# Kernel optimization log

Hardware: AMD Instinct MI355X
Metric: run time of the kernel (lower is better)

Reference implementation:

```python
import jax, jax.numpy as jnp
import numpy as np

D_MODEL = 1024
NUM_HEAD = 16
D_HEAD = 64
EPS = 1e-06


def setup_inputs() -> dict:
    key = jax.random.key(0)
    ks = jax.random.split(key, 16)
    d, h = D_MODEL, 4 * D_MODEL
    s = 1.0 / np.sqrt(d)
    inp = {
        "x": jax.random.normal(ks[0], (8, 1024, d), dtype=jnp.float32),
        # LayerNorm params
        "alpha1": jnp.ones((d,), jnp.float32),
        "beta1": jnp.zeros((d,), jnp.float32),
        "alpha2": jnp.ones((d,), jnp.float32),
        "beta2": jnp.zeros((d,), jnp.float32),
        # attention projections (weights stored as [in, out])
        "w_q": jax.random.normal(ks[1], (d, d), jnp.float32) * s,
        "b_q": jnp.zeros((d,), jnp.float32),
        "w_k": jax.random.normal(ks[2], (d, d), jnp.float32) * s,
        "b_k": jnp.zeros((d,), jnp.float32),
        "w_v": jax.random.normal(ks[3], (d, d), jnp.float32) * s,
        "b_v": jnp.zeros((d,), jnp.float32),
        "w_o": jax.random.normal(ks[4], (d, d), jnp.float32) * s,
        "b_o": jnp.zeros((d,), jnp.float32),
        # MLP
        "w1": jax.random.normal(ks[5], (d, h), jnp.float32) * s,
        "b1": jnp.zeros((h,), jnp.float32),
        "w2": jax.random.normal(ks[6], (h, d), jnp.float32) * (1.0 / np.sqrt(h)),
        "b2": jnp.zeros((d,), jnp.float32),
    }
    return inp


def _layer_norm(x, alpha, beta):
    mu = jnp.mean(x, axis=-1, keepdims=True)
    # torch .var() defaults to unbiased (ddof=1) — replicate exactly
    var = jnp.var(x, axis=-1, keepdims=True, ddof=1)
    return (x - mu) / jnp.sqrt(var + EPS) * alpha + beta


def _mha(x, w_q, b_q, w_k, b_k, w_v, b_v, w_o, b_o):
    b, p, _ = x.shape
    q = (x @ w_q + b_q).reshape(b, p, NUM_HEAD, D_HEAD).transpose(0, 2, 1, 3)
    k = (x @ w_k + b_k).reshape(b, p, NUM_HEAD, D_HEAD).transpose(0, 2, 1, 3)
    v = (x @ w_v + b_v).reshape(b, p, NUM_HEAD, D_HEAD).transpose(0, 2, 1, 3)
    scores = jnp.einsum("bhqd,bhkd->bhqk", q, k) / np.sqrt(D_HEAD).astype(np.float32)
    attn = jax.nn.softmax(scores, axis=-1)
    out = jnp.einsum("bhqk,bhkd->bhqd", attn, v)
    out = out.transpose(0, 2, 1, 3).reshape(b, p, NUM_HEAD * D_HEAD)
    return out @ w_o + b_o


def reference(x, alpha1, beta1, alpha2, beta2,
              w_q, b_q, w_k, b_k, w_v, b_v, w_o, b_o,
              w1, b1, w2, b2):
    # eval mode: Dropout is identity
    x = x + _mha(_layer_norm(x, alpha1, beta1), w_q, b_q, w_k, b_k, w_v, b_v, w_o, b_o)
    h = _layer_norm(x, alpha2, beta2)
    h = jax.nn.gelu(h @ w1 + b1, approximate=False)  # nn.GELU default: exact erf
    h = h @ w2 + b2
    return x + h
```

## Files before the change

kernel.cpp:

```cpp
#include <hip/hip_runtime.h>
#include <stdint.h>

typedef float f32x4 __attribute__((ext_vector_type(4)));
typedef short s16x8 __attribute__((ext_vector_type(8)));
typedef short s16x4 __attribute__((ext_vector_type(4)));
typedef unsigned int u32x4 __attribute__((ext_vector_type(4)));

#define M_TOTAL 8192
#define DM 1024
#define HID 4096
#define SEQ 1024
#define NH 16
#define DH 64

#define BAR() __builtin_amdgcn_s_barrier()
#define VMCNT8() do { asm volatile("s_waitcnt vmcnt(8)" ::: "memory"); __builtin_amdgcn_sched_barrier(0); } while (0)
#define VMCNT0() do { asm volatile("s_waitcnt vmcnt(0)" ::: "memory"); __builtin_amdgcn_sched_barrier(0); } while (0)
#define MFMA16 __builtin_amdgcn_mfma_f32_16x16x32_bf16

__device__ __forceinline__ unsigned short f2bf(float f) {
  unsigned int u = __float_as_uint(f);
  u = (u + 0x7fffu + ((u >> 16) & 1u)) >> 16;
  return (unsigned short)u;
}

__device__ __forceinline__ void gload16(const void* g, void* l) {
  __builtin_amdgcn_global_load_lds((__attribute__((address_space(1))) void*)g,
                                   (__attribute__((address_space(3))) void*)l,
                                   16, 0, 0);
}

__device__ __forceinline__ float erf_fast(float z) {
  const float az = fabsf(z);
  const float tt = 1.0f / fmaf(0.3275911f, az, 1.0f);
  float poly = fmaf(1.061405429f, tt, -1.453152027f);
  poly = fmaf(poly, tt, 1.421413741f);
  poly = fmaf(poly, tt, -0.284496736f);
  poly = fmaf(poly, tt, 0.254829592f);
  poly *= tt;
  const float e = __expf(-az * az);
  const float r = 1.0f - poly * e;
  return (z < 0.f) ? -r : r;
}

__global__ void tcast_all(const float* __restrict__ wq, const float* __restrict__ wk,
                          const float* __restrict__ wv, const float* __restrict__ wo,
                          const float* __restrict__ w1, const float* __restrict__ w2,
                          unsigned short* __restrict__ WTqkv, unsigned short* __restrict__ WTo,
                          unsigned short* __restrict__ WT1, unsigned short* __restrict__ WT2) {
  __shared__ float tile[32][33];
  const int b = blockIdx.x;
  const float* W;
  unsigned short* WT;
  int K, N, bn, bk;
  if (b < 4096) {
    const int j = b >> 10, t2 = b & 1023;
    K = 1024; N = 1024;
    bn = t2 & 31; bk = t2 >> 5;
    W = (j == 0) ? wq : (j == 1) ? wk : (j == 2) ? wv : wo;
    WT = (j < 3) ? (WTqkv + (size_t)j * 1024 * 1024) : WTo;
  } else if (b < 8192) {
    const int t2 = b - 4096;
    K = 1024; N = 4096;
    bn = t2 & 127; bk = t2 >> 7;
    W = w1; WT = WT1;
  } else {
    const int t2 = b - 8192;
    K = 4096; N = 1024;
    bn = t2 & 31; bk = t2 >> 5;
    W = w2; WT = WT2;
  }
  const int tx = threadIdx.x, ty = threadIdx.y;
#pragma unroll
  for (int i = 0; i < 32; i += 8)
    tile[ty + i][tx] = W[(size_t)(bk * 32 + ty + i) * N + bn * 32 + tx];
  __syncthreads();
#pragma unroll
  for (int i = 0; i < 32; i += 8)
    WT[(size_t)(bn * 32 + ty + i) * K + bk * 32 + tx] = f2bf(tile[tx][ty + i]);
}

__global__ __launch_bounds__(256)
void ln_kernel(const float* __restrict__ x, const float* __restrict__ alpha,
               const float* __restrict__ beta, unsigned short* __restrict__ out) {
  const int row = blockIdx.x;
  const int t = threadIdx.x;
  const int w = t >> 6, lane = t & 63;
  const float4 v = ((const float4*)(x + (size_t)row * DM))[t];

  float s = v.x + v.y + v.z + v.w;
#pragma unroll
  for (int off = 32; off; off >>= 1) s += __shfl_xor(s, off, 64);
  __shared__ float red1[4];
  __shared__ float red2[4];
  if (lane == 0) red1[w] = s;
  __syncthreads();
  const float mu = (red1[0] + red1[1] + red1[2] + red1[3]) * (1.f / 1024.f);

  const float dx = v.x - mu, dy = v.y - mu, dz = v.z - mu, dw = v.w - mu;
  float sq = dx * dx + dy * dy + dz * dz + dw * dw;
#pragma unroll
  for (int off = 32; off; off >>= 1) sq += __shfl_xor(sq, off, 64);
  if (lane == 0) red2[w] = sq;
  __syncthreads();
  const float var = (red2[0] + red2[1] + red2[2] + red2[3]) * (1.f / 1023.f);
  const float rstd = rsqrtf(var + 1e-6f);

  const float4 a = ((const float4*)alpha)[t];
  const float4 b = ((const float4*)beta)[t];
  s16x4 o;
  o[0] = (short)f2bf(dx * rstd * a.x + b.x);
  o[1] = (short)f2bf(dy * rstd * a.y + b.y);
  o[2] = (short)f2bf(dz * rstd * a.z + b.z);
  o[3] = (short)f2bf(dw * rstd * a.w + b.w);
  *(s16x4*)(out + (size_t)row * DM + 4 * t) = o;
}

template <int MODE>
__device__ __forceinline__ void epi_store(int m, int n, float v, int Nout,
                                          unsigned short* __restrict__ obf, float* of,
                                          const float* res,
                                          const float* __restrict__ bias0) {
  if (MODE == 1) {
    v += bias0[n] + res[(size_t)m * Nout + n];
    of[(size_t)m * Nout + n] = v;
  } else {
    v += bias0[n];
    const float gv = 0.5f * v * (1.0f + erf_fast(v * 0.70710678118654752f));
    obf[(size_t)m * Nout + n] = f2bf(gv);
  }
}

template <int MODE>
__global__ __launch_bounds__(256, 2)
void gemmk(const unsigned short* __restrict__ A, const unsigned short* __restrict__ B,
           int K, int Nout,
           unsigned short* __restrict__ obf, float* of, const float* res,
           const float* __restrict__ bias0, const float* __restrict__ bias1,
           const float* __restrict__ bias2) {
  __shared__ __attribute__((aligned(16))) unsigned short sA[2][128 * 64];
  __shared__ __attribute__((aligned(16))) unsigned short sB[2][128 * 64];
  const int t = threadIdx.x;
  const int lane = t & 63, wid = t >> 6;
  const int g = lane >> 4, r = lane & 15;
  const int wm = wid >> 1, wn = wid & 1;

  const int L = blockIdx.y * gridDim.x + blockIdx.x;
  const int nwg = gridDim.x * gridDim.y;
  const int chunk = nwg >> 3;
  const int ncols = chunk >> 6;
  const int denom = ncols << 3;
  const int xcd = L & 7, li = L >> 3;
  const int sst = li / denom, wst = li % denom;
  const int by = sst * 8 + (wst & 7);
  const int bx = xcd * ncols + (wst >> 3);
  const int m0 = by * 128, n0 = bx * 128;

  const unsigned short* Ab = A + (size_t)m0 * K;
  const unsigned short* Bb = B + (size_t)n0 * K;

  const int rb = r & 7;
  const int slot0 = (g ^ rb) * 16;
  const int slot1 = ((4 + g) ^ rb) * 16;

  f32x4 acc[4][4];
#pragma unroll
  for (int i2 = 0; i2 < 4; ++i2)
#pragma unroll
    for (int j = 0; j < 4; ++j) acc[i2][j] = (f32x4){0.f, 0.f, 0.f, 0.f};

  auto stage = [&](int buf, int kt) {
#pragma unroll
    for (int s2 = 0; s2 < 4; ++s2) {
      const int f = s2 * 256 + t;
      const int row = f >> 3, c = f & 7;
      const int u = c ^ (row & 7);
      gload16(Ab + (size_t)row * K + kt * 64 + u * 8, &sA[buf][(size_t)row * 64 + c * 8]);
      gload16(Bb + (size_t)row * K + kt * 64 + u * 8, &sB[buf][(size_t)row * 64 + c * 8]);
    }
  };

  const int NT = K >> 6;
  stage(0, 0);
  stage(1, (NT > 1) ? 1 : 0);
  VMCNT8();
  BAR();

  for (int tt = 0; tt < NT; ++tt) {
    const int cur = tt & 1;
    const char* sAc = (const char*)&sA[cur][0];
    const char* sBc = (const char*)&sB[cur][0];

    s16x8 av[4][2], bv[4][2];
#pragma unroll
    for (int i2 = 0; i2 < 4; ++i2) {
      const int rbyte = (wm * 64 + i2 * 16 + r) * 128;
      av[i2][0] = *(const s16x8*)(sAc + rbyte + slot0);
      av[i2][1] = *(const s16x8*)(sAc + rbyte + slot1);
    }
#pragma unroll
    for (int n = 0; n < 4; ++n) {
      const int rbyte = (wn * 64 + n * 16 + r) * 128;
      bv[n][0] = *(const s16x8*)(sBc + rbyte + slot0);
      bv[n][1] = *(const s16x8*)(sBc + rbyte + slot1);
    }
#pragma unroll
    for (int i2 = 0; i2 < 4; ++i2)
#pragma unroll
      for (int n = 0; n < 4; ++n) {
        acc[i2][n] = MFMA16(av[i2][0], bv[n][0], acc[i2][n], 0, 0, 0);
        acc[i2][n] = MFMA16(av[i2][1], bv[n][1], acc[i2][n], 0, 0, 0);
      }

    BAR();
    const int tp2 = (tt + 2 < NT) ? tt + 2 : NT - 1;
    stage(cur, tp2);
    VMCNT8();
    BAR();
  }

  VMCNT0();

  if (MODE == 0) {
#pragma unroll
    for (int i2 = 0; i2 < 4; ++i2)
#pragma unroll
      for (int nf = 0; nf < 4; ++nf) {
        const int n = n0 + wn * 64 + nf * 16 + r;
        const int which = n >> 10, nn = n & 1023;
        const int h = nn >> 6, d = nn & 63;
        const int m_base = m0 + wm * 64 + i2 * 16 + 4 * g;
        const int b = m_base >> 10, s_base = m_base & 1023;
        if (which == 2) {
          const float bias = bias2[nn];
          s16x4 o;
#pragma unroll
          for (int j = 0; j < 4; ++j) o[j] = (short)f2bf(acc[i2][nf][j] + bias);
          *(s16x4*)(obf + (size_t)2 * (M_TOTAL * DM) +
                    (((size_t)(b * NH + h) * DH + d) * SEQ + s_base)) = o;
        } else {
          const float bias = (which == 0) ? bias0[nn] : bias1[nn];
#pragma unroll
          for (int j = 0; j < 4; ++j) {
            float v = acc[i2][nf][j] + bias;
            if (which == 0) v *= 0.125f;
            obf[(size_t)which * (M_TOTAL * DM) +
                (((size_t)(b * NH + h) * SEQ + (s_base + j)) * DH + d)] = f2bf(v);
          }
        }
      }
  } else {
#pragma unroll
    for (int i2 = 0; i2 < 4; ++i2)
#pragma unroll
      for (int j = 0; j < 4; ++j) {
        const int m = m0 + wm * 64 + i2 * 16 + 4 * g + j;
#pragma unroll
        for (int nf = 0; nf < 4; ++nf) {
          const int n = n0 + wn * 64 + nf * 16 + r;
          epi_store<MODE>(m, n, acc[i2][nf][j], Nout, obf, of, res, bias0);
        }
      }
  }
}

__global__ __launch_bounds__(256)
void attn_kernel(const unsigned short* __restrict__ QKV,
                 unsigned short* __restrict__ O) {
  const unsigned short* Qg = QKV;
  const unsigned short* Kg = QKV + (size_t)M_TOTAL * DM;
  const unsigned short* VTg = QKV + 2 * (size_t)M_TOTAL * DM;
  const int bh = blockIdx.y;
  const int q0 = blockIdx.x * 64;
  const int t = threadIdx.x, w = t >> 6, lane = t & 63;
  const int g = lane >> 4, r = lane & 15;
  const unsigned short* Qb = Qg + (size_t)bh * SEQ * DH;
  const unsigned short* Kb = Kg + (size_t)bh * SEQ * DH;
  const unsigned short* VTb = VTg + (size_t)bh * DH * SEQ;

  __shared__ __attribute__((aligned(16))) unsigned short sK[2][64 * 64];
  __shared__ __attribute__((aligned(16))) unsigned short sV[2][64 * 64];

  s16x8 qf[2];
  {
    const unsigned short* qrow = Qb + (size_t)(q0 + w * 16 + r) * DH;
    qf[0] = *(const s16x8*)(qrow + g * 8);
    qf[1] = *(const s16x8*)(qrow + 32 + g * 8);
  }

  f32x4 oacc[4];
#pragma unroll
  for (int i = 0; i < 4; ++i) oacc[i] = (f32x4){0.f, 0.f, 0.f, 0.f};
  float mrun = -1e30f, lrun = 0.f;

  auto stage = [&](int buf, int kt) {
#pragma unroll
    for (int s2 = 0; s2 < 2; ++s2) {
      const int f = s2 * 256 + t;
      const int row = f >> 3, u = (f & 7) ^ (row & 7);
      gload16(Kb + (size_t)(kt * 64 + row) * DH + u * 8, &sK[buf][f * 8]);
      gload16(VTb + (size_t)row * SEQ + kt * 64 + u * 8, &sV[buf][f * 8]);
    }
  };

  stage(0, 0);
  __syncthreads();

  for (int kt = 0; kt < SEQ / 64; ++kt) {
    const int cur = kt & 1;
    if (kt < SEQ / 64 - 1) stage(cur ^ 1, kt + 1);

    f32x4 sc[4];
#pragma unroll
    for (int nf = 0; nf < 4; ++nf) {
      sc[nf] = (f32x4){0.f, 0.f, 0.f, 0.f};
      const int rowk = nf * 16 + r;
#pragma unroll
      for (int ks = 0; ks < 2; ++ks) {
        const int u = (4 * ks + g) ^ (rowk & 7);
        const s16x8 kf = *(const s16x8*)&sK[cur][rowk * 64 + u * 8];
        sc[nf] = __builtin_amdgcn_mfma_f32_16x16x32_bf16(kf, qf[ks], sc[nf], 0, 0, 0);
      }
    }

    float pm = -1e30f;
#pragma unroll
    for (int nf = 0; nf < 4; ++nf)
#pragma unroll
      for (int j = 0; j < 4; ++j) pm = fmaxf(pm, sc[nf][j]);
    pm = fmaxf(pm, __shfl_xor(pm, 16, 64));
    pm = fmaxf(pm, __shfl_xor(pm, 32, 64));

    const float mnew = fmaxf(mrun, pm);
    const float alpha = __expf(mrun - mnew);
    mrun = mnew;

    float p[4][4];
    float ps = 0.f;
#pragma unroll
    for (int nf = 0; nf < 4; ++nf)
#pragma unroll
      for (int j = 0; j < 4; ++j) {
        p[nf][j] = __expf(sc[nf][j] - mnew);
        ps += p[nf][j];
      }
    ps += __shfl_xor(ps, 16, 64);
    ps += __shfl_xor(ps, 32, 64);
    lrun = lrun * alpha + ps;

    float ao[4];
#pragma unroll
    for (int j = 0; j < 4; ++j) ao[j] = __shfl(alpha, 4 * g + j, 64);
#pragma unroll
    for (int nf2 = 0; nf2 < 4; ++nf2)
#pragma unroll
      for (int j = 0; j < 4; ++j) oacc[nf2][j] *= ao[j];

    unsigned int pk[4][2];
#pragma unroll
    for (int nf = 0; nf < 4; ++nf)
#pragma unroll
      for (int jp = 0; jp < 2; ++jp)
        pk[nf][jp] = (unsigned int)f2bf(p[nf][2 * jp]) |
                     ((unsigned int)f2bf(p[nf][2 * jp + 1]) << 16);

    unsigned int pa32[2][4];
#pragma unroll
    for (int ks = 0; ks < 2; ++ks)
#pragma unroll
      for (int q2 = 0; q2 < 4; ++q2) {
        const int src = r + 32 * (g & 1) + 16 * (q2 >> 1);
        const unsigned int a = (unsigned int)__shfl((int)pk[2 * ks][q2 & 1], src, 64);
        const unsigned int b = (unsigned int)__shfl((int)pk[2 * ks + 1][q2 & 1], src, 64);
        pa32[ks][q2] = (g >> 1) ? b : a;
      }
    s16x8 pa[2];
#pragma unroll
    for (int ks = 0; ks < 2; ++ks) {
      u32x4 pw;
      pw[0] = pa32[ks][0]; pw[1] = pa32[ks][1];
      pw[2] = pa32[ks][2]; pw[3] = pa32[ks][3];
      pa[ks] = __builtin_bit_cast(s16x8, pw);
    }

#pragma unroll
    for (int nf2 = 0; nf2 < 4; ++nf2) {
      const int rowd = nf2 * 16 + r;
#pragma unroll
      for (int ks = 0; ks < 2; ++ks) {
        const int u = (4 * ks + g) ^ (rowd & 7);
        const s16x8 vb = *(const s16x8*)&sV[cur][rowd * 64 + u * 8];
        oacc[nf2] = __builtin_amdgcn_mfma_f32_16x16x32_bf16(pa[ks], vb, oacc[nf2], 0, 0, 0);
      }
    }
    __syncthreads();
  }

  const int b = bh >> 4, h = bh & 15;
  const float linv = 1.f / lrun;
#pragma unroll
  for (int j = 0; j < 4; ++j) {
    const float lo = __shfl(linv, 4 * g + j, 64);
    const int q = q0 + w * 16 + 4 * g + j;
    const size_t orow = ((size_t)(b * SEQ + q)) * DM + h * DH;
#pragma unroll
    for (int nf2 = 0; nf2 < 4; ++nf2)
      O[orow + nf2 * 16 + r] = f2bf(oacc[nf2][j] * lo);
  }
}

extern "C" void kernel_launch(void* const* d_in, const int* in_sizes, int n_in,
                              void* d_out, int out_size, void* d_ws, size_t ws_size,
                              hipStream_t stream) {
  const float* x   = (const float*)d_in[0];
  const float* al1 = (const float*)d_in[1];
  const float* be1 = (const float*)d_in[2];
  const float* al2 = (const float*)d_in[3];
  const float* be2 = (const float*)d_in[4];
  const float* wq  = (const float*)d_in[5];
  const float* bq  = (const float*)d_in[6];
  const float* wk  = (const float*)d_in[7];
  const float* bk  = (const float*)d_in[8];
  const float* wv  = (const float*)d_in[9];
  const float* bv  = (const float*)d_in[10];
  const float* wo  = (const float*)d_in[11];
  const float* bo  = (const float*)d_in[12];
  const float* w1  = (const float*)d_in[13];
  const float* b1  = (const float*)d_in[14];
  const float* w2  = (const float*)d_in[15];
  const float* b2  = (const float*)d_in[16];
  float* dout = (float*)d_out;

  unsigned short* ws = (unsigned short*)d_ws;
  size_t off = 0;
  auto alloc = [&](size_t n) { unsigned short* p = ws + off; off += n; return p; };
  unsigned short* WTqkv = alloc((size_t)3072 * 1024);
  unsigned short* WTo   = alloc((size_t)1024 * 1024);
  unsigned short* WT1   = alloc((size_t)4096 * 1024);
  unsigned short* WT2   = alloc((size_t)1024 * 4096);
  unsigned short* xn    = alloc((size_t)M_TOTAL * DM);
  unsigned short* QKVb  = alloc((size_t)3 * M_TOTAL * DM);
  unsigned short* attn  = alloc((size_t)M_TOTAL * DM);
  unsigned short* h1    = alloc((size_t)M_TOTAL * HID);
  (void)ws_size; (void)in_sizes; (void)n_in; (void)out_size;

  tcast_all<<<12288, dim3(32, 8), 0, stream>>>(wq, wk, wv, wo, w1, w2,
                                               WTqkv, WTo, WT1, WT2);

  ln_kernel<<<M_TOTAL, 256, 0, stream>>>(x, al1, be1, xn);
  gemmk<0><<<dim3(24, 64), 256, 0, stream>>>(xn, WTqkv, 1024, 3072,
                                             QKVb, nullptr, nullptr, bq, bk, bv);
  attn_kernel<<<dim3(16, 128), 256, 0, stream>>>(QKVb, attn);
  gemmk<1><<<dim3(8, 64), 256, 0, stream>>>(attn, WTo, 1024, 1024,
                                            nullptr, dout, x, bo, nullptr, nullptr);
  ln_kernel<<<M_TOTAL, 256, 0, stream>>>(dout, al2, be2, xn);
  gemmk<2><<<dim3(32, 64), 256, 0, stream>>>(xn, WT1, 1024, 4096,
                                             h1, nullptr, nullptr, b1, nullptr, nullptr);
  gemmk<1><<<dim3(8, 64), 256, 0, stream>>>(h1, WT2, 4096, 1024,
                                            nullptr, dout, dout, b2, nullptr, nullptr);
}
```

Baseline: 419.0 us.

## Stage V-transpose epilogue through LDS and add lazy softmax rescaling in attention

The QKV projection epilogue for the V slice now writes each wave's 64x64 tile into shared memory, then reads it back transposed so global stores to the d-major V layout are contiguous 8-byte runs along the sequence. Previously these were scattered 4-element stores. Q/K epilogue indexing is also simplified by hoisting the head and batch computation per wave. Separately, the flash-attention loop only rescales the running max, sum and output accumulators when some lane's new max exceeds the old by more than 8, which skips exp and shuffle work on most iterations but lets probabilities grow up to e^8 before rescaling.

```diff
diff --git a/kernel.cpp b/kernel.cpp
--- a/kernel.cpp
+++ b/kernel.cpp
@@ -222,33 +222,49 @@
   VMCNT0();
 
   if (MODE == 0) {
-#pragma unroll
-    for (int i2 = 0; i2 < 4; ++i2)
-#pragma unroll
-      for (int nf = 0; nf < 4; ++nf) {
-        const int n = n0 + wn * 64 + nf * 16 + r;
-        const int which = n >> 10, nn = n & 1023;
-        const int h = nn >> 6, d = nn & 63;
-        const int m_base = m0 + wm * 64 + i2 * 16 + 4 * g;
-        const int b = m_base >> 10, s_base = m_base & 1023;
-        if (which == 2) {
-          const float bias = bias2[nn];
+    const int which = n0 >> 10;
+    const int hn = ((n0 & 1023) + wn * 64) >> 6;
+    const int mwave = m0 + wm * 64;
+    const int b = mwave >> 10, s_wb = mwave & 1023;
+    if (which == 2) {
+      BAR();
+      unsigned short* tl = (unsigned short*)&sA[0][0] + (size_t)wid * (64 * 64);
+#pragma unroll
+      for (int i2 = 0; i2 < 4; ++i2)
+#pragma unroll
+        for (int nf = 0; nf < 4; ++nf) {
+          const int d = nf * 16 + r;
+          const float bias = bias2[hn * 64 + d];
           s16x4 o;
 #pragma unroll
           for (int j = 0; j < 4; ++j) o[j] = (short)f2bf(acc[i2][nf][j] + bias);
-          *(s16x4*)(obf + (size_t)2 * (M_TOTAL * DM) +
-                    (((size_t)(b * NH + h) * DH + d) * SEQ + s_base)) = o;
-        } else {
-          const float bias = (which == 0) ? bias0[nn] : bias1[nn];
+          *(s16x4*)&tl[d * 64 + i2 * 16 + 4 * g] = o;
+        }
+      unsigned short* vout = obf + (size_t)2 * (M_TOTAL * DM) +
+                             ((size_t)(b * NH + hn) * DH) * SEQ + s_wb;
+#pragma unroll
+      for (int p2 = 0; p2 < 16; ++p2) {
+        const int d = p2 * 4 + g;
+        const s16x4 v = *(const s16x4*)&tl[d * 64 + 4 * r];
+        *(s16x4*)(vout + (size_t)d * SEQ + 4 * r) = v;
+      }
+    } else {
+#pragma unroll
+      for (int i2 = 0; i2 < 4; ++i2)
+#pragma unroll
+        for (int nf = 0; nf < 4; ++nf) {
+          const int d = nf * 16 + r;
+          const float bias = (which == 0) ? bias0[hn * 64 + d] : bias1[hn * 64 + d];
+          const int s_base = s_wb + i2 * 16 + 4 * g;
 #pragma unroll
           for (int j = 0; j < 4; ++j) {
             float v = acc[i2][nf][j] + bias;
             if (which == 0) v *= 0.125f;
             obf[(size_t)which * (M_TOTAL * DM) +
-                (((size_t)(b * NH + h) * SEQ + (s_base + j)) * DH + d)] = f2bf(v);
+                (((size_t)(b * NH + hn) * SEQ + (s_base + j)) * DH + d)] = f2bf(v);
           }
         }
-      }
+    }
   } else {
 #pragma unroll
     for (int i2 = 0; i2 < 4; ++i2)
@@ -331,9 +347,19 @@
     pm = fmaxf(pm, __shfl_xor(pm, 16, 64));
     pm = fmaxf(pm, __shfl_xor(pm, 32, 64));
 
-    const float mnew = fmaxf(mrun, pm);
-    const float alpha = __expf(mrun - mnew);
-    mrun = mnew;
+    if (!__all(pm - mrun <= 8.0f)) {
+      const float mnew = fmaxf(mrun, pm);
+      const float alpha = __expf(mrun - mnew);
+      mrun = mnew;
+      lrun *= alpha;
+      float ao[4];
+#pragma unroll
+      for (int j = 0; j < 4; ++j) ao[j] = __shfl(alpha, 4 * g + j, 64);
+#pragma unroll
+      for (int nf2 = 0; nf2 < 4; ++nf2)
+#pragma unroll
+        for (int j = 0; j < 4; ++j) oacc[nf2][j] *= ao[j];
+    }
 
     float p[4][4];
     float ps = 0.f;
@@ -341,20 +367,12 @@
     for (int nf = 0; nf < 4; ++nf)
 #pragma unroll
       for (int j = 0; j < 4; ++j) {
-        p[nf][j] = __expf(sc[nf][j] - mnew);
+        p[nf][j] = __expf(sc[nf][j] - mrun);
         ps += p[nf][j];
       }
     ps += __shfl_xor(ps, 16, 64);
     ps += __shfl_xor(ps, 32, 64);
-    lrun = lrun * alpha + ps;
-
-    float ao[4];
-#pragma unroll
-    for (int j = 0; j < 4; ++j) ao[j] = __shfl(alpha, 4 * g + j, 64);
-#pragma unroll
-    for (int nf2 = 0; nf2 < 4; ++nf2)
-#pragma unroll
-      for (int j = 0; j < 4; ++j) oacc[nf2][j] *= ao[j];
+    lrun += ps;
 
     unsigned int pk[4][2];
 #pragma unroll
```

Result: faster. 408.2 us (-2.6%).
